# Optimization experiments

Hardware: AMD Instinct MI355X
Metric: run time of the kernel (lower is better)

## Reference

```python
import jax, jax.numpy as jnp
import numpy as np

N_NODES = 100000
N_EDGES = 1600000
N_GRAPHS = 1024
HID = 128
NODE_DIM = 7
EDGE_DIM = 3
LAYERS = 4
LN_EPS = 1e-5


def setup_inputs() -> dict:
    key = jax.random.key(0)
    ks = jax.random.split(key, 24)
    s = lambda i, shape, scale=0.05: (jax.random.normal(ks[i], shape, dtype=jnp.float32) * scale)
    x = jax.random.normal(ks[0], (N_NODES, NODE_DIM), dtype=jnp.float32)
    edge_index = jax.random.randint(ks[1], (2, N_EDGES), 0, N_NODES, dtype=jnp.int32)
    edge_attr = jax.random.normal(ks[2], (N_EDGES, EDGE_DIM), dtype=jnp.float32)
    batch = jnp.sort(jax.random.randint(ks[3], (N_NODES,), 0, N_GRAPHS, dtype=jnp.int32))
    return {
        'x': x, 'edge_index': edge_index, 'edge_attr': edge_attr, 'batch': batch,
        'inW': s(4, (NODE_DIM, HID)), 'inb': s(5, (HID,)),
        'edgeW': s(6, (LAYERS, EDGE_DIM, HID)), 'edgeb': s(7, (LAYERS, HID)),
        'w1': s(8, (LAYERS, HID, HID)), 'b1': s(9, (LAYERS, HID)),
        'w2': s(10, (LAYERS, HID, HID)), 'b2': s(11, (LAYERS, HID)),
        'gamma': jnp.ones((LAYERS, HID), dtype=jnp.float32),
        'beta': jnp.zeros((LAYERS, HID), dtype=jnp.float32),
        'fcW1': s(12, (HID, HID)), 'fcb1': s(13, (HID,)),
        'fcW2': s(14, (HID, HID // 2)), 'fcb2': s(15, (HID // 2,)),
        'fcW3': s(16, (HID // 2, 1)), 'fcb3': s(17, (1,)),
    }


def _layernorm(x, gamma, beta):
    mu = jnp.mean(x, axis=-1, keepdims=True)
    var = jnp.mean(jnp.square(x - mu), axis=-1, keepdims=True)
    return (x - mu) * jax.lax.rsqrt(var + LN_EPS) * gamma + beta


def reference(x, edge_index, edge_attr, batch, inW, inb, edgeW, edgeb,
              w1, b1, w2, b2, gamma, beta, fcW1, fcb1, fcW2, fcb2, fcW3, fcb3):
    src, dst = edge_index[0], edge_index[1]
    h = x @ inW + inb  # [N, HID]
    for l in range(LAYERS):
        e = edge_attr @ edgeW[l] + edgeb[l]              # [E, HID]
        msg = jax.nn.relu(h[src] + e)                    # gather + relu
        agg = jax.ops.segment_sum(msg, dst, num_segments=N_NODES)  # scatter-add
        g = agg + h                                      # (1+eps)*x_r with eps=0
        g = jax.nn.relu(g @ w1[l] + b1[l]) @ w2[l] + b2[l]  # GINE MLP
        h = _layernorm(h + jax.nn.relu(g), gamma[l], beta[l])  # residual + LN
    # global mean pool over graphs
    sums = jax.ops.segment_sum(h, batch, num_segments=N_GRAPHS)
    cnt = jax.ops.segment_sum(jnp.ones((h.shape[0],), h.dtype), batch, num_segments=N_GRAPHS)
    pooled = sums / jnp.maximum(cnt, 1.0)[:, None]
    # head (dropout is identity in eval)
    o = jax.nn.relu(pooled @ fcW1 + fcb1)
    o = jax.nn.relu(o @ fcW2 + fcb2)
    return o @ fcW3 + fcb3  # [N_GRAPHS, 1]
```

## Files before the change

### kernel.cpp

```cpp
#include <hip/hip_runtime.h>

#define N_NODES 100000
#define N_EDGES 1600000
#define N_GRAPHS 1024
#define HID 128
#define LAYERS 4
#define LN_EPS 1e-5f
#define NB_SCAN 391
#define GTS 136
#define NB_PROJ 50000
#define NB_WCONV 512

typedef __attribute__((ext_vector_type(8))) short bf16x8;
typedef __attribute__((ext_vector_type(4))) float f32x4;

__device__ __forceinline__ unsigned short f2bf(float x) {
    unsigned v = __float_as_uint(x);
    return (unsigned short)((v + 0x7fffu + ((v >> 16) & 1u)) >> 16);
}
__device__ __forceinline__ float bfval(unsigned short u) {
    return __uint_as_float((unsigned)u << 16);
}

__global__ __launch_bounds__(256) void k_prep(
    const float* __restrict__ x, const float* __restrict__ inW,
    const float* __restrict__ inb, float* __restrict__ h,
    unsigned short* __restrict__ hb,
    const float* __restrict__ w1, const float* __restrict__ w2,
    unsigned short* __restrict__ wf_hi, unsigned short* __restrict__ wf_lo) {
    if (blockIdx.x < NB_PROJ) {
        int idx = blockIdx.x * 256 + threadIdx.x;
        int n = idx >> 7, c = idx & 127;
        const float* xr = x + n * 7;
        float s = inb[c];
#pragma unroll
        for (int k = 0; k < 7; ++k) s += xr[k] * inW[k * HID + c];
        h[idx] = s;
        hb[idx] = f2bf(s);
    } else {
        int idx = (blockIdx.x - NB_PROJ) * 256 + threadIdx.x;
        int wid = idx >> 14;
        int layer = wid >> 1, which = wid & 1;
        int within = idx & 16383;
        int nt = within >> 11;
        int ks = (within >> 9) & 3;
        int ln = (within >> 3) & 63;
        int j = within & 7;
        const float* W = (which ? w2 : w1) + layer * HID * HID;
        int k = ks * 32 + (ln >> 4) * 8 + j;
        int n = nt * 16 + (ln & 15);
        float v = W[k * HID + n];
        unsigned short hi = f2bf(v);
        wf_hi[idx] = hi;
        wf_lo[idx] = f2bf(v - bfval(hi));
    }
}

__global__ __launch_bounds__(256) void k_hist(
    const int* __restrict__ ei, int* __restrict__ deg) {
    int e = blockIdx.x * 256 + threadIdx.x;
    atomicAdd(&deg[ei[N_EDGES + e]], 1);
}

__global__ __launch_bounds__(256) void k_scan1(
    const int* __restrict__ deg, int* __restrict__ bsum) {
    const int i = blockIdx.x * 256 + threadIdx.x;
    int v = (i < N_NODES) ? deg[i] : 0;
#pragma unroll
    for (int off = 1; off < 64; off <<= 1) v += __shfl_xor(v, off);
    __shared__ int wsum[4];
    if ((threadIdx.x & 63) == 0) wsum[threadIdx.x >> 6] = v;
    __syncthreads();
    if (threadIdx.x == 0) bsum[blockIdx.x] = wsum[0] + wsum[1] + wsum[2] + wsum[3];
}

__global__ __launch_bounds__(512) void k_scan2(
    const int* __restrict__ bsum, int* __restrict__ bpre) {
    __shared__ int tmp[512];
    const int t = threadIdx.x;
    int v = (t < NB_SCAN) ? bsum[t] : 0;
    tmp[t] = v;
    __syncthreads();
    for (int off = 1; off < 512; off <<= 1) {
        int u = (t >= off) ? tmp[t - off] : 0;
        __syncthreads();
        tmp[t] += u;
        __syncthreads();
    }
    if (t < NB_SCAN) bpre[t] = tmp[t] - v;
}

__global__ __launch_bounds__(256) void k_scan3(
    const int* __restrict__ deg, const int* __restrict__ bpre,
    int* __restrict__ row_ptr, int* __restrict__ cursor) {
    __shared__ int tmp[256];
    const int t = threadIdx.x;
    const int i = blockIdx.x * 256 + t;
    int d = (i < N_NODES) ? deg[i] : 0;
    tmp[t] = d;
    __syncthreads();
    for (int off = 1; off < 256; off <<= 1) {
        int u = (t >= off) ? tmp[t - off] : 0;
        __syncthreads();
        tmp[t] += u;
        __syncthreads();
    }
    if (i < N_NODES) {
        const int ex = bpre[blockIdx.x] + tmp[t] - d;
        row_ptr[i] = ex;
        cursor[i] = ex;
        if (i == N_NODES - 1) row_ptr[N_NODES] = N_EDGES;
    }
}

__global__ __launch_bounds__(256) void k_scatter(
    const int* __restrict__ ei, const float* __restrict__ ea,
    int* __restrict__ cursor, float4* __restrict__ edata) {
    int e = blockIdx.x * 256 + threadIdx.x;
    const int src = ei[e];
    const int dst = ei[N_EDGES + e];
    const int pos = atomicAdd(&cursor[dst], 1);
    edata[pos] = make_float4(ea[e * 3 + 0], ea[e * 3 + 1], ea[e * 3 + 2],
                             __int_as_float(src));
}

#define EL(JJ)                                                                 \
    const int s##JJ = __builtin_amdgcn_readfirstlane(                          \
        __float_as_int(etile[wbase + (j + JJ) * 4 + 3]));                      \
    const unsigned gq##JJ = *(const unsigned*)(hbin + (long)s##JJ * HID + c2);

#define EC(JJ) {                                                               \
    const float4 ed = *(const float4*)&etile[wbase + (j + JJ) * 4];            \
    const float gx = __uint_as_float(gq##JJ << 16) + ebv.x;                    \
    const float gy = __uint_as_float(gq##JJ & 0xffff0000u) + ebv.y;            \
    const float mx = fmaxf(fmaf(ed.z, ew2.x, fmaf(ed.y, ew1.x,                 \
                     fmaf(ed.x, ew0.x, gx))), 0.f);                            \
    const float my = fmaxf(fmaf(ed.z, ew2.y, fmaf(ed.y, ew1.y,                 \
                     fmaf(ed.x, ew0.y, gy))), 0.f);                            \
    const int gi = t + j + (JJ);                                               \
    if (gi < rp1)      { a0x += mx; a0y += my; }                               \
    else if (gi < rp2) { a1x += mx; a1y += my; }                               \
    else if (gi < rp3) { a2x += mx; a2y += my; }                               \
    else               { a3x += mx; a3y += my; } }

#define ROW_OUT(R, AX, AY) {                                                   \
    const float2 hv = *(const float2*)(h + (long)(nb + (R)) * HID + c2);       \
    const float gx = hv.x + (AX), gy = hv.y + (AY);                            \
    const unsigned short hx = f2bf(gx), hy = f2bf(gy);                         \
    const unsigned short lx = f2bf(gx - bfval(hx)), ly = f2bf(gy - bfval(hy)); \
    *(unsigned*)&gt_hi[(r0 + (R)) * GTS + c2] = (unsigned)hx | ((unsigned)hy << 16); \
    *(unsigned*)&gt_lo[(r0 + (R)) * GTS + c2] = (unsigned)lx | ((unsigned)ly << 16); }

#define T1_OUT(CC, NT) {                                                       \
    const float4 bv = *(const float4*)(b1 + (NT) * 16 + q4);                   \
    const float v0 = fmaxf(CC[0] + bv.x, 0.f);                                 \
    const float v1 = fmaxf(CC[1] + bv.y, 0.f);                                 \
    const float v2 = fmaxf(CC[2] + bv.z, 0.f);                                 \
    const float v3 = fmaxf(CC[3] + bv.w, 0.f);                                 \
    const unsigned short h0_ = f2bf(v0), h1_ = f2bf(v1), h2_ = f2bf(v2), h3_ = f2bf(v3); \
    const unsigned short l0_ = f2bf(v0 - bfval(h0_)), l1_ = f2bf(v1 - bfval(h1_)); \
    const unsigned short l2_ = f2bf(v2 - bfval(h2_)), l3_ = f2bf(v3 - bfval(h3_)); \
    *(uint2*)&t1_hi[ln15 * GTS + (NT) * 16 + q4] =                             \
        make_uint2((unsigned)h0_ | ((unsigned)h1_ << 16), (unsigned)h2_ | ((unsigned)h3_ << 16)); \
    *(uint2*)&t1_lo[ln15 * GTS + (NT) * 16 + q4] =                             \
        make_uint2((unsigned)l0_ | ((unsigned)l1_ << 16), (unsigned)l2_ | ((unsigned)l3_ << 16)); }

__global__ __launch_bounds__(256, 6) void k_node_update(
    const float4* __restrict__ edata, const int* __restrict__ row_ptr,
    const float* __restrict__ eW, const float* __restrict__ eb,
    float* __restrict__ h, const unsigned short* __restrict__ hbin,
    unsigned short* __restrict__ hbout,
    const unsigned short* __restrict__ w1f_hi, const unsigned short* __restrict__ w1f_lo,
    const unsigned short* __restrict__ w2f_hi, const unsigned short* __restrict__ w2f_lo,
    const float* __restrict__ b1, const float* __restrict__ b2,
    const float* __restrict__ gamma, const float* __restrict__ beta) {
    __shared__ __align__(16) unsigned char smem[21504];
    float* etile = (float*)smem;
    float* stats = (float*)smem;
    unsigned short* gt_hi = (unsigned short*)(smem + 4096);
    unsigned short* gt_lo = (unsigned short*)(smem + 8448);
    unsigned short* t1_hi = (unsigned short*)(smem + 12800);
    unsigned short* t1_lo = (unsigned short*)(smem + 17152);

    const int wave = threadIdx.x >> 6;
    const int lane = threadIdx.x & 63;
    const int n0 = blockIdx.x * 16;
    const int r0 = wave * 4;
    const int c2 = lane * 2;
    const int wbase = wave * 256;

    {
        const float2 ew0 = *(const float2*)(eW + 0 * HID + c2);
        const float2 ew1 = *(const float2*)(eW + 1 * HID + c2);
        const float2 ew2 = *(const float2*)(eW + 2 * HID + c2);
        const float2 ebv = *(const float2*)(eb + c2);
        const int nb = n0 + r0;
        const int rp0 = __builtin_amdgcn_readfirstlane(row_ptr[nb + 0]);
        const int rp1 = __builtin_amdgcn_readfirstlane(row_ptr[nb + 1]);
        const int rp2 = __builtin_amdgcn_readfirstlane(row_ptr[nb + 2]);
        const int rp3 = __builtin_amdgcn_readfirstlane(row_ptr[nb + 3]);
        const int rp4 = __builtin_amdgcn_readfirstlane(row_ptr[nb + 4]);

        float a0x = 0.f, a0y = 0.f, a1x = 0.f, a1y = 0.f;
        float a2x = 0.f, a2y = 0.f, a3x = 0.f, a3y = 0.f;

        float4 cur;
        if (rp0 + lane < rp4) cur = edata[rp0 + lane];
        for (int t = rp0; t < rp4; t += 64) {
            const int cnt = (rp4 - t < 64) ? (rp4 - t) : 64;
            if (lane < cnt)
                *(float4*)&etile[wbase + lane * 4] = cur;
            if (t + 64 + lane < rp4) cur = edata[t + 64 + lane];
            int j = 0;
            for (; j + 16 <= cnt; j += 16) {
                EL(0) EL(1) EL(2) EL(3) EL(4) EL(5) EL(6) EL(7)
                EL(8) EL(9) EL(10) EL(11) EL(12) EL(13) EL(14) EL(15)
                EC(0) EC(1) EC(2) EC(3) EC(4) EC(5) EC(6) EC(7)
                EC(8) EC(9) EC(10) EC(11) EC(12) EC(13) EC(14) EC(15)
            }
            for (; j + 4 <= cnt; j += 4) {
                EL(0) EL(1) EL(2) EL(3)
                EC(0) EC(1) EC(2) EC(3)
            }
            for (; j < cnt; ++j) {
                EL(0)
                EC(0)
            }
        }
        ROW_OUT(0, a0x, a0y)
        ROW_OUT(1, a1x, a1y)
        ROW_OUT(2, a2x, a2y)
        ROW_OUT(3, a3x, a3y)
    }
    __syncthreads();

    const int ln15 = lane & 15;
    const int q8 = (lane >> 4) * 8;
    const int q4 = (lane >> 4) * 4;
    const int nt0 = wave * 2, nt1 = nt0 + 1;

    {
        f32x4 c0 = {0.f, 0.f, 0.f, 0.f};
        f32x4 c1 = {0.f, 0.f, 0.f, 0.f};
#pragma unroll
        for (int ks = 0; ks < 4; ++ks) {
            const bf16x8 bh = *(const bf16x8*)&gt_hi[ln15 * GTS + ks * 32 + q8];
            const bf16x8 bl = *(const bf16x8*)&gt_lo[ln15 * GTS + ks * 32 + q8];
            const bf16x8 a0h = *(const bf16x8*)(w1f_hi + (((nt0 * 4 + ks) * 64 + lane) << 3));
            const bf16x8 a0l = *(const bf16x8*)(w1f_lo + (((nt0 * 4 + ks) * 64 + lane) << 3));
            const bf16x8 a1h = *(const bf16x8*)(w1f_hi + (((nt1 * 4 + ks) * 64 + lane) << 3));
            const bf16x8 a1l = *(const bf16x8*)(w1f_lo + (((nt1 * 4 + ks) * 64 + lane) << 3));
            c0 = __builtin_amdgcn_mfma_f32_16x16x32_bf16(a0h, bh, c0, 0, 0, 0);
            c0 = __builtin_amdgcn_mfma_f32_16x16x32_bf16(a0h, bl, c0, 0, 0, 0);
            c0 = __builtin_amdgcn_mfma_f32_16x16x32_bf16(a0l, bh, c0, 0, 0, 0);
            c1 = __builtin_amdgcn_mfma_f32_16x16x32_bf16(a1h, bh, c1, 0, 0, 0);
            c1 = __builtin_amdgcn_mfma_f32_16x16x32_bf16(a1h, bl, c1, 0, 0, 0);
            c1 = __builtin_amdgcn_mfma_f32_16x16x32_bf16(a1l, bh, c1, 0, 0, 0);
        }
        T1_OUT(c0, nt0)
        T1_OUT(c1, nt1)
    }
    __syncthreads();

    {
        f32x4 c0 = {0.f, 0.f, 0.f, 0.f};
        f32x4 c1 = {0.f, 0.f, 0.f, 0.f};
#pragma unroll
        for (int ks = 0; ks < 4; ++ks) {
            const bf16x8 bh = *(const bf16x8*)&t1_hi[ln15 * GTS + ks * 32 + q8];
            const bf16x8 bl = *(const bf16x8*)&t1_lo[ln15 * GTS + ks * 32 + q8];
            const bf16x8 a0h = *(const bf16x8*)(w2f_hi + (((nt0 * 4 + ks) * 64 + lane) << 3));
            const bf16x8 a0l = *(const bf16x8*)(w2f_lo + (((nt0 * 4 + ks) * 64 + lane) << 3));
            const bf16x8 a1h = *(const bf16x8*)(w2f_hi + (((nt1 * 4 + ks) * 64 + lane) << 3));
            const bf16x8 a1l = *(const bf16x8*)(w2f_lo + (((nt1 * 4 + ks) * 64 + lane) << 3));
            c0 = __builtin_amdgcn_mfma_f32_16x16x32_bf16(a0h, bh, c0, 0, 0, 0);
            c0 = __builtin_amdgcn_mfma_f32_16x16x32_bf16(a0h, bl, c0, 0, 0, 0);
            c0 = __builtin_amdgcn_mfma_f32_16x16x32_bf16(a0l, bh, c0, 0, 0, 0);
            c1 = __builtin_amdgcn_mfma_f32_16x16x32_bf16(a1h, bh, c1, 0, 0, 0);
            c1 = __builtin_amdgcn_mfma_f32_16x16x32_bf16(a1h, bl, c1, 0, 0, 0);
            c1 = __builtin_amdgcn_mfma_f32_16x16x32_bf16(a1l, bh, c1, 0, 0, 0);
        }
        const int row = n0 + ln15;
        const float4 b20 = *(const float4*)(b2 + nt0 * 16 + q4);
        const float4 b21 = *(const float4*)(b2 + nt1 * 16 + q4);
        const float4 hv0 = *(const float4*)(h + (long)row * HID + nt0 * 16 + q4);
        const float4 hv1 = *(const float4*)(h + (long)row * HID + nt1 * 16 + q4);
        float4 u0, u1;
        u0.x = hv0.x + fmaxf(c0[0] + b20.x, 0.f);
        u0.y = hv0.y + fmaxf(c0[1] + b20.y, 0.f);
        u0.z = hv0.z + fmaxf(c0[2] + b20.z, 0.f);
        u0.w = hv0.w + fmaxf(c0[3] + b20.w, 0.f);
        u1.x = hv1.x + fmaxf(c1[0] + b21.x, 0.f);
        u1.y = hv1.y + fmaxf(c1[1] + b21.y, 0.f);
        u1.z = hv1.z + fmaxf(c1[2] + b21.z, 0.f);
        u1.w = hv1.w + fmaxf(c1[3] + b21.w, 0.f);
        float s = u0.x + u0.y + u0.z + u0.w + u1.x + u1.y + u1.z + u1.w;
        float s2 = u0.x * u0.x + u0.y * u0.y + u0.z * u0.z + u0.w * u0.w +
                   u1.x * u1.x + u1.y * u1.y + u1.z * u1.z + u1.w * u1.w;
        s += __shfl_xor(s, 16); s2 += __shfl_xor(s2, 16);
        s += __shfl_xor(s, 32); s2 += __shfl_xor(s2, 32);
        if (lane < 16) {
            stats[wave * 32 + lane * 2 + 0] = s;
            stats[wave * 32 + lane * 2 + 1] = s2;
        }
        __syncthreads();
        const float S  = stats[0 * 32 + ln15 * 2] + stats[1 * 32 + ln15 * 2] +
                         stats[2 * 32 + ln15 * 2] + stats[3 * 32 + ln15 * 2];
        const float S2 = stats[0 * 32 + ln15 * 2 + 1] + stats[1 * 32 + ln15 * 2 + 1] +
                         stats[2 * 32 + ln15 * 2 + 1] + stats[3 * 32 + ln15 * 2 + 1];
        const float mu = S * (1.f / HID);
        const float var = S2 * (1.f / HID) - mu * mu;
        const float inv = rsqrtf(var + LN_EPS);
        const float4 gm0 = *(const float4*)(gamma + nt0 * 16 + q4);
        const float4 gm1 = *(const float4*)(gamma + nt1 * 16 + q4);
        const float4 bt0 = *(const float4*)(beta + nt0 * 16 + q4);
        const float4 bt1 = *(const float4*)(beta + nt1 * 16 + q4);
        float4 o0, o1;
        o0.x = (u0.x - mu) * inv * gm0.x + bt0.x;
        o0.y = (u0.y - mu) * inv * gm0.y + bt0.y;
        o0.z = (u0.z - mu) * inv * gm0.z + bt0.z;
        o0.w = (u0.w - mu) * inv * gm0.w + bt0.w;
        o1.x = (u1.x - mu) * inv * gm1.x + bt1.x;
        o1.y = (u1.y - mu) * inv * gm1.y + bt1.y;
        o1.z = (u1.z - mu) * inv * gm1.z + bt1.z;
        o1.w = (u1.w - mu) * inv * gm1.w + bt1.w;
        *(float4*)(h + (long)row * HID + nt0 * 16 + q4) = o0;
        *(float4*)(h + (long)row * HID + nt1 * 16 + q4) = o1;
        *(uint2*)(hbout + (long)row * HID + nt0 * 16 + q4) =
            make_uint2((unsigned)f2bf(o0.x) | ((unsigned)f2bf(o0.y) << 16),
                       (unsigned)f2bf(o0.z) | ((unsigned)f2bf(o0.w) << 16));
        *(uint2*)(hbout + (long)row * HID + nt1 * 16 + q4) =
            make_uint2((unsigned)f2bf(o1.x) | ((unsigned)f2bf(o1.y) << 16),
                       (unsigned)f2bf(o1.z) | ((unsigned)f2bf(o1.w) << 16));
    }
}

__global__ __launch_bounds__(128) void k_pool(
    const float* __restrict__ h, const int* __restrict__ batch,
    float* __restrict__ sums, float* __restrict__ cnt) {
    const int c = threadIdx.x;
    const int n0 = blockIdx.x * 64;
    if (n0 >= N_NODES) return;
    const int nend = min(n0 + 64, N_NODES);
    int cur = batch[n0];
    float acc = 0.f;
    int runlen = 0;
    for (int n = n0; n < nend; ++n) {
        const int b = batch[n];
        if (b != cur) {
            atomicAdd(&sums[(long)cur * HID + c], acc);
            if (c == 0) atomicAdd(&cnt[cur], (float)runlen);
            acc = 0.f;
            runlen = 0;
            cur = b;
        }
        acc += h[(long)n * HID + c];
        ++runlen;
    }
    atomicAdd(&sums[(long)cur * HID + c], acc);
    if (c == 0) atomicAdd(&cnt[cur], (float)runlen);
}

__global__ __launch_bounds__(128) void k_head(
    const float* __restrict__ sums, const float* __restrict__ cnt,
    const float* __restrict__ fcW1, const float* __restrict__ fcb1,
    const float* __restrict__ fcW2, const float* __restrict__ fcb2,
    const float* __restrict__ fcW3, const float* __restrict__ fcb3,
    float* __restrict__ out) {
    __shared__ float p[HID];
    __shared__ float o1[HID];
    __shared__ float o2[64];
    const int g = blockIdx.x, t = threadIdx.x;
    const float c = fmaxf(cnt[g], 1.0f);
    p[t] = sums[g * HID + t] / c;
    __syncthreads();
    float s = fcb1[t];
    for (int k = 0; k < HID; ++k) s += p[k] * fcW1[k * HID + t];
    o1[t] = fmaxf(s, 0.f);
    __syncthreads();
    if (t < 64) {
        float s2 = fcb2[t];
        for (int k = 0; k < HID; ++k) s2 += o1[k] * fcW2[k * 64 + t];
        o2[t] = fmaxf(s2, 0.f);
    }
    __syncthreads();
    if (t < 64) {
        float v = o2[t] * fcW3[t];
#pragma unroll
        for (int off = 32; off > 0; off >>= 1) v += __shfl_down(v, off);
        if (t == 0) out[g] = v + fcb3[0];
    }
}

extern "C" void kernel_launch(void* const* d_in, const int* in_sizes, int n_in,
                              void* d_out, int out_size, void* d_ws, size_t ws_size,
                              hipStream_t stream) {
    const float* x    = (const float*)d_in[0];
    const int*   ei   = (const int*)d_in[1];
    const float* ea   = (const float*)d_in[2];
    const int*   batch= (const int*)d_in[3];
    const float* inW  = (const float*)d_in[4];
    const float* inb  = (const float*)d_in[5];
    const float* edgeW= (const float*)d_in[6];
    const float* edgeb= (const float*)d_in[7];
    const float* w1   = (const float*)d_in[8];
    const float* b1   = (const float*)d_in[9];
    const float* w2   = (const float*)d_in[10];
    const float* b2   = (const float*)d_in[11];
    const float* gamma= (const float*)d_in[12];
    const float* beta = (const float*)d_in[13];
    const float* fcW1 = (const float*)d_in[14];
    const float* fcb1 = (const float*)d_in[15];
    const float* fcW2 = (const float*)d_in[16];
    const float* fcb2 = (const float*)d_in[17];
    const float* fcW3 = (const float*)d_in[18];
    const float* fcb3 = (const float*)d_in[19];
    float* out = (float*)d_out;

    float4* edata = (float4*)d_ws;
    float*  h     = (float*)(edata + N_EDGES);
    unsigned short* hb0 = (unsigned short*)(h + (size_t)N_NODES * HID);
    unsigned short* hb1 = hb0 + (size_t)N_NODES * HID;
    unsigned short* wf_hi = hb1 + (size_t)N_NODES * HID;
    unsigned short* wf_lo = wf_hi + LAYERS * 2 * 16384;
    int*    row_ptr = (int*)(wf_lo + LAYERS * 2 * 16384);
    int*    cursor  = row_ptr + (N_NODES + 1);
    int*    deg     = cursor + N_NODES;
    int*    bsum    = deg + N_NODES;
    int*    bpre    = bsum + 512;
    float*  sums    = (float*)(bpre + 512);
    float*  cnt     = sums + (size_t)N_GRAPHS * HID;

    hipMemsetAsync(deg, 0, N_NODES * sizeof(int), stream);
    hipMemsetAsync(sums, 0, ((size_t)N_GRAPHS * HID + N_GRAPHS) * sizeof(float), stream);

    k_prep<<<NB_PROJ + NB_WCONV, 256, 0, stream>>>(x, inW, inb, h, hb0,
                                                   w1, w2, wf_hi, wf_lo);

    k_hist<<<N_EDGES / 256, 256, 0, stream>>>(ei, deg);
    k_scan1<<<NB_SCAN, 256, 0, stream>>>(deg, bsum);
    k_scan2<<<1, 512, 0, stream>>>(bsum, bpre);
    k_scan3<<<NB_SCAN, 256, 0, stream>>>(deg, bpre, row_ptr, cursor);
    k_scatter<<<N_EDGES / 256, 256, 0, stream>>>(ei, ea, cursor, edata);

    unsigned short* hbin = hb0;
    unsigned short* hbout = hb1;
    for (int l = 0; l < LAYERS; ++l) {
        k_node_update<<<N_NODES / 16, 256, 0, stream>>>(
            edata, row_ptr, edgeW + l * 3 * HID, edgeb + l * HID,
            h, hbin, hbout,
            wf_hi + (l * 2 + 0) * 16384, wf_lo + (l * 2 + 0) * 16384,
            wf_hi + (l * 2 + 1) * 16384, wf_lo + (l * 2 + 1) * 16384,
            b1 + l * HID, b2 + l * HID, gamma + l * HID, beta + l * HID);
        unsigned short* tmp = hbin; hbin = hbout; hbout = tmp;
    }

    k_pool<<<(N_NODES + 63) / 64, 128, 0, stream>>>(h, batch, sums, cnt);
    k_head<<<N_GRAPHS, 128, 0, stream>>>(sums, cnt, fcW1, fcb1, fcW2, fcb2,
                                         fcW3, fcb3, out);
}
```

Before: 789.7 us.

## Fuse histogram and block sums into prep; read edge data via readlane instead of LDS

```diff
diff --git a/kernel.cpp b/kernel.cpp
--- a/kernel.cpp
+++ b/kernel.cpp
@@ -10,6 +10,7 @@
 #define GTS 136
 #define NB_PROJ 50000
 #define NB_WCONV 512
+#define NB_HIST 6250
 
 typedef __attribute__((ext_vector_type(8))) short bf16x8;
 typedef __attribute__((ext_vector_type(4))) float f32x4;
@@ -27,7 +28,8 @@
     const float* __restrict__ inb, float* __restrict__ h,
     unsigned short* __restrict__ hb,
     const float* __restrict__ w1, const float* __restrict__ w2,
-    unsigned short* __restrict__ wf_hi, unsigned short* __restrict__ wf_lo) {
+    unsigned short* __restrict__ wf_hi, unsigned short* __restrict__ wf_lo,
+    const int* __restrict__ ei, int* __restrict__ deg, int* __restrict__ bsum) {
     if (blockIdx.x < NB_PROJ) {
         int idx = blockIdx.x * 256 + threadIdx.x;
         int n = idx >> 7, c = idx & 127;
@@ -37,7 +39,7 @@
         for (int k = 0; k < 7; ++k) s += xr[k] * inW[k * HID + c];
         h[idx] = s;
         hb[idx] = f2bf(s);
-    } else {
+    } else if (blockIdx.x < NB_PROJ + NB_WCONV) {
         int idx = (blockIdx.x - NB_PROJ) * 256 + threadIdx.x;
         int wid = idx >> 14;
         int layer = wid >> 1, which = wid & 1;
@@ -53,25 +55,12 @@
         unsigned short hi = f2bf(v);
         wf_hi[idx] = hi;
         wf_lo[idx] = f2bf(v - bfval(hi));
-    }
-}
-
-__global__ __launch_bounds__(256) void k_hist(
-    const int* __restrict__ ei, int* __restrict__ deg) {
-    int e = blockIdx.x * 256 + threadIdx.x;
-    atomicAdd(&deg[ei[N_EDGES + e]], 1);
-}
-
-__global__ __launch_bounds__(256) void k_scan1(
-    const int* __restrict__ deg, int* __restrict__ bsum) {
-    const int i = blockIdx.x * 256 + threadIdx.x;
-    int v = (i < N_NODES) ? deg[i] : 0;
-#pragma unroll
-    for (int off = 1; off < 64; off <<= 1) v += __shfl_xor(v, off);
-    __shared__ int wsum[4];
-    if ((threadIdx.x & 63) == 0) wsum[threadIdx.x >> 6] = v;
-    __syncthreads();
-    if (threadIdx.x == 0) bsum[blockIdx.x] = wsum[0] + wsum[1] + wsum[2] + wsum[3];
+    } else {
+        int e = (blockIdx.x - NB_PROJ - NB_WCONV) * 256 + threadIdx.x;
+        const int dst = ei[N_EDGES + e];
+        atomicAdd(&deg[dst], 1);
+        atomicAdd(&bsum[dst >> 8], 1);
+    }
 }
 
 __global__ __launch_bounds__(512) void k_scan2(
@@ -125,18 +114,17 @@
 }
 
 #define EL(JJ)                                                                 \
-    const int s##JJ = __builtin_amdgcn_readfirstlane(                          \
-        __float_as_int(etile[wbase + (j + JJ) * 4 + 3]));                      \
+    const int s##JJ = __builtin_amdgcn_readlane(__float_as_int(cur.w), j + JJ); \
     const unsigned gq##JJ = *(const unsigned*)(hbin + (long)s##JJ * HID + c2);
 
 #define EC(JJ) {                                                               \
-    const float4 ed = *(const float4*)&etile[wbase + (j + JJ) * 4];            \
+    const float ax_ = __uint_as_float(__builtin_amdgcn_readlane(__float_as_int(cur.x), j + JJ)); \
+    const float ay_ = __uint_as_float(__builtin_amdgcn_readlane(__float_as_int(cur.y), j + JJ)); \
+    const float az_ = __uint_as_float(__builtin_amdgcn_readlane(__float_as_int(cur.z), j + JJ)); \
     const float gx = __uint_as_float(gq##JJ << 16) + ebv.x;                    \
     const float gy = __uint_as_float(gq##JJ & 0xffff0000u) + ebv.y;            \
-    const float mx = fmaxf(fmaf(ed.z, ew2.x, fmaf(ed.y, ew1.x,                 \
-                     fmaf(ed.x, ew0.x, gx))), 0.f);                            \
-    const float my = fmaxf(fmaf(ed.z, ew2.y, fmaf(ed.y, ew1.y,                 \
-                     fmaf(ed.x, ew0.y, gy))), 0.f);                            \
+    const float mx = fmaxf(fmaf(az_, ew2.x, fmaf(ay_, ew1.x, fmaf(ax_, ew0.x, gx))), 0.f); \
+    const float my = fmaxf(fmaf(az_, ew2.y, fmaf(ay_, ew1.y, fmaf(ax_, ew0.y, gy))), 0.f); \
     const int gi = t + j + (JJ);                                               \
     if (gi < rp1)      { a0x += mx; a0y += my; }                               \
     else if (gi < rp2) { a1x += mx; a1y += my; }                               \
@@ -165,7 +153,7 @@
     *(uint2*)&t1_lo[ln15 * GTS + (NT) * 16 + q4] =                             \
         make_uint2((unsigned)l0_ | ((unsigned)l1_ << 16), (unsigned)l2_ | ((unsigned)l3_ << 16)); }
 
-__global__ __launch_bounds__(256, 6) void k_node_update(
+__global__ __launch_bounds__(256, 8) void k_node_update(
     const float4* __restrict__ edata, const int* __restrict__ row_ptr,
     const float* __restrict__ eW, const float* __restrict__ eb,
     float* __restrict__ h, const unsigned short* __restrict__ hbin,
@@ -174,20 +162,18 @@
     const unsigned short* __restrict__ w2f_hi, const unsigned short* __restrict__ w2f_lo,
     const float* __restrict__ b1, const float* __restrict__ b2,
     const float* __restrict__ gamma, const float* __restrict__ beta) {
-    __shared__ __align__(16) unsigned char smem[21504];
-    float* etile = (float*)smem;
+    __shared__ __align__(16) unsigned char smem[17408];
     float* stats = (float*)smem;
-    unsigned short* gt_hi = (unsigned short*)(smem + 4096);
-    unsigned short* gt_lo = (unsigned short*)(smem + 8448);
-    unsigned short* t1_hi = (unsigned short*)(smem + 12800);
-    unsigned short* t1_lo = (unsigned short*)(smem + 17152);
+    unsigned short* gt_hi = (unsigned short*)(smem + 0);
+    unsigned short* gt_lo = (unsigned short*)(smem + 4352);
+    unsigned short* t1_hi = (unsigned short*)(smem + 8704);
+    unsigned short* t1_lo = (unsigned short*)(smem + 13056);
 
     const int wave = threadIdx.x >> 6;
     const int lane = threadIdx.x & 63;
     const int n0 = blockIdx.x * 16;
     const int r0 = wave * 4;
     const int c2 = lane * 2;
-    const int wbase = wave * 256;
 
     {
         const float2 ew0 = *(const float2*)(eW + 0 * HID + c2);
@@ -204,13 +190,11 @@
         float a0x = 0.f, a0y = 0.f, a1x = 0.f, a1y = 0.f;
         float a2x = 0.f, a2y = 0.f, a3x = 0.f, a3y = 0.f;
 
-        float4 cur;
+        float4 cur, nxt;
         if (rp0 + lane < rp4) cur = edata[rp0 + lane];
         for (int t = rp0; t < rp4; t += 64) {
             const int cnt = (rp4 - t < 64) ? (rp4 - t) : 64;
-            if (lane < cnt)
-                *(float4*)&etile[wbase + lane * 4] = cur;
-            if (t + 64 + lane < rp4) cur = edata[t + 64 + lane];
+            if (t + 64 + lane < rp4) nxt = edata[t + 64 + lane];
             int j = 0;
             for (; j + 16 <= cnt; j += 16) {
                 EL(0) EL(1) EL(2) EL(3) EL(4) EL(5) EL(6) EL(7)
@@ -226,6 +210,7 @@
                 EL(0)
                 EC(0)
             }
+            cur = nxt;
         }
         ROW_OUT(0, a0x, a0y)
         ROW_OUT(1, a1x, a1y)
@@ -430,15 +415,14 @@
     int*    bpre    = bsum + 512;
     float*  sums    = (float*)(bpre + 512);
     float*  cnt     = sums + (size_t)N_GRAPHS * HID;
-
-    hipMemsetAsync(deg, 0, N_NODES * sizeof(int), stream);
-    hipMemsetAsync(sums, 0, ((size_t)N_GRAPHS * HID + N_GRAPHS) * sizeof(float), stream);
-
-    k_prep<<<NB_PROJ + NB_WCONV, 256, 0, stream>>>(x, inW, inb, h, hb0,
-                                                   w1, w2, wf_hi, wf_lo);
-
-    k_hist<<<N_EDGES / 256, 256, 0, stream>>>(ei, deg);
-    k_scan1<<<NB_SCAN, 256, 0, stream>>>(deg, bsum);
+    const size_t zbytes = (N_NODES + 512 + 512) * sizeof(int) +
+                          ((size_t)N_GRAPHS * HID + N_GRAPHS) * sizeof(float);
+
+    hipMemsetAsync(deg, 0, zbytes, stream);
+
+    k_prep<<<NB_PROJ + NB_WCONV + NB_HIST, 256, 0, stream>>>(
+        x, inW, inb, h, hb0, w1, w2, wf_hi, wf_lo, ei, deg, bsum);
+
     k_scan2<<<1, 512, 0, stream>>>(bsum, bpre);
     k_scan3<<<NB_SCAN, 256, 0, stream>>>(deg, bpre, row_ptr, cursor);
     k_scatter<<<N_EDGES / 256, 256, 0, stream>>>(ei, ea, cursor, edata);
```

Result: slower. 1.298 ms (+64.4%).
